# Performance work log

Hardware: AMD Instinct MI355X
Metric: run time of the kernel (lower is better)

The kernel has to match this reference:

```python
import jax, jax.numpy as jnp
import numpy as np

N = 50000        # nodes
E = 1600000      # edges (before self loops)
D_IN = 768       # roberta-base hidden size
SIZES = [256, 256]
NEG_SLOPE = 0.2
EPS = 1e-16


def setup_inputs() -> dict:
    key = jax.random.key(0)
    ks = jax.random.split(key, 16)
    s = 0.05
    inp = {
        "x": jax.random.normal(ks[0], (N, D_IN), dtype=jnp.float32),
        "edge_index": jax.random.randint(ks[1], (2, E), 0, N, dtype=jnp.int64),
        # GAT layer 0
        "W0": jax.random.normal(ks[2], (D_IN, SIZES[0]), dtype=jnp.float32) * s,
        "a_src0": jax.random.normal(ks[3], (SIZES[0],), dtype=jnp.float32) * s,
        "a_dst0": jax.random.normal(ks[4], (SIZES[0],), dtype=jnp.float32) * s,
        "b0": jnp.zeros((SIZES[0],), dtype=jnp.float32),
        # GAT layer 1
        "W1": jax.random.normal(ks[5], (SIZES[0], SIZES[1]), dtype=jnp.float32) * s,
        "a_src1": jax.random.normal(ks[6], (SIZES[1],), dtype=jnp.float32) * s,
        "a_dst1": jax.random.normal(ks[7], (SIZES[1],), dtype=jnp.float32) * s,
        "b1": jnp.zeros((SIZES[1],), dtype=jnp.float32),
        # GlobalAttention gate_nn: Linear(256 -> 1)
        "gate_w": jax.random.normal(ks[8], (SIZES[1], 1), dtype=jnp.float32) * s,
        "gate_b": jnp.zeros((1,), dtype=jnp.float32),
    }
    return inp


def _gat_layer(x, src, dst, W, a_src, a_dst, b):
    # PyG GATConv, heads=1: h = x W; e_ij = leaky_relu(a_src.h_j + a_dst.h_i)
    # softmax over edges grouped by target node i, then weighted aggregation.
    h = x @ W                                   # [N, D]
    alpha_src = h @ a_src                       # [N]
    alpha_dst = h @ a_dst                       # [N]
    e = jax.nn.leaky_relu(alpha_src[src] + alpha_dst[dst], NEG_SLOPE)  # [E']
    e_max = jax.ops.segment_max(e, dst, num_segments=N)
    e = jnp.exp(e - e_max[dst])
    denom = jax.ops.segment_sum(e, dst, num_segments=N)
    alpha = e / (denom[dst] + EPS)              # [E'] softmax per target
    out = jax.ops.segment_sum(alpha[:, None] * h[src], dst, num_segments=N)
    return out + b


def reference(x, edge_index, W0, a_src0, a_dst0, b0, W1, a_src1, a_dst1, b1, gate_w, gate_b):
    # add self loops (GATConv default add_self_loops=True)
    loop = jnp.arange(N, dtype=edge_index.dtype)
    src = jnp.concatenate([edge_index[0], loop])
    dst = jnp.concatenate([edge_index[1], loop])

    h = jax.nn.relu(_gat_layer(x, src, dst, W0, a_src0, a_dst0, b0))
    h = jax.nn.relu(_gat_layer(h, src, dst, W1, a_src1, a_dst1, b1))

    # GlobalAttention pooling over the single graph
    gate = h @ gate_w + gate_b                  # [N, 1]
    attn = jax.nn.softmax(gate, axis=0)         # softmax over nodes
    out = jnp.sum(attn * h, axis=0, keepdims=True)  # [1, 256]
    return out
```

## Files before the change

kernel.cpp:

```cpp
#include <hip/hip_runtime.h>

typedef unsigned int uint;
typedef unsigned short u16;
typedef unsigned char u8;

typedef __attribute__((ext_vector_type(8))) short short8;
typedef __attribute__((ext_vector_type(8))) u16 u16x8;
typedef __attribute__((ext_vector_type(4))) float f32x4;
typedef __attribute__((ext_vector_type(2))) float f32x2;

#define NN 50000
#define EE 1600000
#define ETOT (EE + NN)
#define NBUCK 782
#define ACHUNK 8192
#define CAP 2432
#define NSLOT 64
#define SLOTW 260

__device__ __forceinline__ u16 f2bf(float f) {
  uint u = __builtin_bit_cast(uint, f);
  uint r = u + 0x7fffu + ((u >> 16) & 1u);
  return (u16)(r >> 16);
}
__device__ __forceinline__ float bf2f(u16 h) {
  return __builtin_bit_cast(float, ((uint)h) << 16);
}
__device__ __forceinline__ u8 f2fp8(float f) {
  int t = __builtin_amdgcn_cvt_pk_fp8_f32(f, f, 0, false);
  return (u8)(t & 0xff);
}
__device__ __forceinline__ float wred_sum(float v) {
#pragma unroll
  for (int off = 32; off > 0; off >>= 1) v += __shfl_xor(v, off);
  return v;
}

__global__ void zero_ws(uint* __restrict__ bnxt, float* __restrict__ slots) {
  int i = blockIdx.x * 256 + threadIdx.x;
  if (i < NBUCK) bnxt[i] = 0u;
  if (i < NSLOT * SLOTW) slots[i] = 0.f;
}

__global__ void wt_both(const float* __restrict__ W0, const float* __restrict__ W1,
                        u16* __restrict__ Wt0, u16* __restrict__ Wt1) {
  int i = blockIdx.x * 256 + threadIdx.x;
  if (i < 768 * 256) {
    int k = i >> 8, n = i & 255;
    Wt0[n * 768 + k] = f2bf(W0[i]);
  } else if (i < 768 * 256 + 256 * 256) {
    int j = i - 768 * 256;
    int k = j >> 8, n = j & 255;
    Wt1[n * 256 + k] = f2bf(W1[j]);
  }
}

template <bool ABF16>
__global__ __launch_bounds__(512) void gemm_fused(const void* __restrict__ Avoid,
                                                  const u16* __restrict__ Bt,
                                                  u8* __restrict__ C8,
                                                  const float* __restrict__ a_src,
                                                  const float* __restrict__ a_dst,
                                                  float* __restrict__ as_,
                                                  float* __restrict__ ad_,
                                                  int M, int K) {
  __shared__ __align__(16) u16 As[128 * 64];
  __shared__ __align__(16) u16 Bs[256 * 64];
  __shared__ float asLds[4][128];
  __shared__ float adLds[4][128];
  const int m0 = blockIdx.x * 128;
  const int tid = threadIdx.x;
  const int lane = tid & 63;
  const int wv = tid >> 6;
  const int wm = wv >> 2, wn = wv & 3;

  f32x4 acc[4][4] = {};

  const int sr = tid >> 2;
  const int skc = (tid & 3) * 16;
  const int br = tid >> 1;
  const int bk = (tid & 1) * 32;

  for (int k0 = 0; k0 < K; k0 += 64) {
    {
      int grow = m0 + sr;
      if constexpr (!ABF16) {
        const float* A = (const float*)Avoid;
        float4 f[4];
        if (grow < M) {
          const float4* src = reinterpret_cast<const float4*>(A + (size_t)grow * K + k0 + skc);
#pragma unroll
          for (int i = 0; i < 4; ++i) f[i] = src[i];
        } else {
#pragma unroll
          for (int i = 0; i < 4; ++i) f[i] = make_float4(0.f, 0.f, 0.f, 0.f);
        }
#pragma unroll
        for (int i = 0; i < 2; ++i) {
          u16x8 v;
          v[0] = f2bf(f[2 * i].x); v[1] = f2bf(f[2 * i].y);
          v[2] = f2bf(f[2 * i].z); v[3] = f2bf(f[2 * i].w);
          v[4] = f2bf(f[2 * i + 1].x); v[5] = f2bf(f[2 * i + 1].y);
          v[6] = f2bf(f[2 * i + 1].z); v[7] = f2bf(f[2 * i + 1].w);
          int k = skc + i * 8;
          int idx = (sr << 6) + (k ^ ((sr & 7) << 3));
          *reinterpret_cast<u16x8*>(&As[idx]) = v;
        }
      } else {
        const u16* A = (const u16*)Avoid;
        u16x8 v[2];
        if (grow < M) {
          const u16x8* src = reinterpret_cast<const u16x8*>(A + (size_t)grow * K + k0 + skc);
          v[0] = src[0]; v[1] = src[1];
        } else {
          v[0] = (u16x8)0; v[1] = (u16x8)0;
        }
#pragma unroll
        for (int i = 0; i < 2; ++i) {
          int k = skc + i * 8;
          int idx = (sr << 6) + (k ^ ((sr & 7) << 3));
          *reinterpret_cast<u16x8*>(&As[idx]) = v[i];
        }
      }
    }
    {
      const u16x8* src = reinterpret_cast<const u16x8*>(Bt + (size_t)br * K + k0 + bk);
#pragma unroll
      for (int i = 0; i < 4; ++i) {
        u16x8 v = src[i];
        int k = bk + i * 8;
        int idx = (br << 6) + (k ^ ((br & 7) << 3));
        *reinterpret_cast<u16x8*>(&Bs[idx]) = v;
      }
    }
    __syncthreads();
#pragma unroll
    for (int kk = 0; kk < 2; ++kk) {
      short8 af[4], bfr[4];
      const int kb = kk * 32 + (lane >> 4) * 8;
#pragma unroll
      for (int m = 0; m < 4; ++m) {
        int r = wm * 64 + m * 16 + (lane & 15);
        int idx = (r << 6) + (kb ^ ((r & 7) << 3));
        af[m] = *reinterpret_cast<const short8*>(&As[idx]);
      }
#pragma unroll
      for (int n = 0; n < 4; ++n) {
        int c = wn * 64 + n * 16 + (lane & 15);
        int idx = (c << 6) + (kb ^ ((c & 7) << 3));
        bfr[n] = *reinterpret_cast<const short8*>(&Bs[idx]);
      }
#pragma unroll
      for (int m = 0; m < 4; ++m)
#pragma unroll
        for (int n = 0; n < 4; ++n)
          acc[m][n] = __builtin_amdgcn_mfma_f32_16x16x32_bf16(af[m], bfr[n], acc[m][n], 0, 0, 0);
    }
    __syncthreads();
  }

  const int g = lane >> 4;
  const int cl = lane & 15;
  float asv[4], adv[4];
#pragma unroll
  for (int n = 0; n < 4; ++n) {
    int c = wn * 64 + n * 16 + cl;
    asv[n] = a_src[c];
    adv[n] = a_dst[c];
  }
#pragma unroll
  for (int m = 0; m < 4; ++m) {
#pragma unroll
    for (int reg = 0; reg < 4; ++reg) {
      int rl = wm * 64 + m * 16 + g * 4 + reg;
      int row = m0 + rl;
      float ps = 0.f, pd = 0.f;
      if (row < M) {
#pragma unroll
        for (int n = 0; n < 4; ++n) {
          float v = acc[m][n][reg];
          C8[(size_t)row * 256 + wn * 64 + n * 16 + cl] = f2fp8(v);
          ps = fmaf(v, asv[n], ps);
          pd = fmaf(v, adv[n], pd);
        }
      }
#pragma unroll
      for (int off = 1; off < 16; off <<= 1) {
        ps += __shfl_xor(ps, off);
        pd += __shfl_xor(pd, off);
      }
      if (cl == 0) {
        asLds[wn][rl] = ps;
        adLds[wn][rl] = pd;
      }
    }
  }
  __syncthreads();
  if (tid < 128) {
    int row = m0 + tid;
    if (row < M) {
      as_[row] = asLds[0][tid] + asLds[1][tid] + asLds[2][tid] + asLds[3][tid];
      ad_[row] = adLds[0][tid] + adLds[1][tid] + adLds[2][tid] + adLds[3][tid];
    }
  }
}

__global__ __launch_bounds__(256) void bucket_scatter(const int* __restrict__ esrc,
                                                      const int* __restrict__ edst,
                                                      uint* __restrict__ bnxt,
                                                      uint* __restrict__ tmp) {
  __shared__ uint lh[NBUCK];
  int base = blockIdx.x * ACHUNK;
  int nE = ETOT - base; if (nE > ACHUNK) nE = ACHUNK;
  for (int i = threadIdx.x; i < NBUCK; i += 256) lh[i] = 0;
  __syncthreads();
  for (int k = threadIdx.x; k < nE; k += 256) {
    int e = base + k;
    int d = (e < EE) ? edst[e] : (e - EE);
    atomicAdd(&lh[d >> 6], 1u);
  }
  __syncthreads();
  for (int i = threadIdx.x; i < NBUCK; i += 256) {
    uint c = lh[i];
    lh[i] = c ? atomicAdd(&bnxt[i], c) : 0u;
  }
  __syncthreads();
  for (int k = threadIdx.x; k < nE; k += 256) {
    int e = base + k;
    int s, d;
    if (e < EE) { s = esrc[e]; d = edst[e]; } else { s = e - EE; d = s; }
    uint pos = atomicAdd(&lh[d >> 6], 1u);
    tmp[(size_t)(d >> 6) * CAP + pos] = ((uint)(d & 63) << 16) | (uint)s;
  }
}

__global__ __launch_bounds__(1024) void scanb_kernel(const uint* __restrict__ bnxt,
                                                     uint* __restrict__ bptr) {
  __shared__ uint wsum[16];
  int tid = threadIdx.x, lane = tid & 63, w = tid >> 6;
  uint v = (tid < NBUCK) ? bnxt[tid] : 0u;
  uint x = v;
#pragma unroll
  for (int off = 1; off < 64; off <<= 1) {
    uint t = __shfl_up(x, off);
    if (lane >= off) x += t;
  }
  if (lane == 63) wsum[w] = x;
  __syncthreads();
  uint woff = 0;
  for (int k = 0; k < w; ++k) woff += wsum[k];
  uint excl = woff + x - v;
  if (tid < NBUCK) bptr[tid] = excl;
}

__global__ __launch_bounds__(256) void bucket_sort(const uint* __restrict__ tmp,
                                                   const uint* __restrict__ bptr,
                                                   const uint* __restrict__ bnxt,
                                                   uint* __restrict__ row_ptr,
                                                   u16* __restrict__ csr) {
  __shared__ uint lh[64];
  __shared__ uint buf[CAP];
  int b = blockIdx.x;
  uint s0 = bptr[b];
  int cnt = (int)bnxt[b];
  int tid = threadIdx.x;
  if (tid < 64) lh[tid] = 0;
  __syncthreads();
  for (int i = tid; i < cnt; i += 256) {
    uint v = tmp[(size_t)b * CAP + i];
    buf[i] = v;
    atomicAdd(&lh[v >> 16], 1u);
  }
  __syncthreads();
  if (tid < 64) {
    uint v = lh[tid];
    uint x = v;
#pragma unroll
    for (int off = 1; off < 64; off <<= 1) {
      uint t = __shfl_up(x, off);
      if (tid >= off) x += t;
    }
    uint pos = s0 + x - v;
    int d = b * 64 + tid;
    if (d < NN) row_ptr[d] = pos;
    lh[tid] = pos;
    if (b == NBUCK - 1 && tid == 0) row_ptr[NN] = s0 + (uint)cnt;
  }
  __syncthreads();
  for (int i = tid; i < cnt; i += 256) {
    uint v = buf[i];
    uint pos = atomicAdd(&lh[v >> 16], 1u);
    csr[pos] = (u16)(v & 0xFFFFu);
  }
}

#define FMA16(v, wg)                                                                   \
  do {                                                                                 \
    f32x2 p_;                                                                          \
    p_ = __builtin_amdgcn_cvt_pk_f32_fp8((v).x, false);                                \
    acc[0] = fmaf((wg), p_.x, acc[0]); acc[1] = fmaf((wg), p_.y, acc[1]);              \
    p_ = __builtin_amdgcn_cvt_pk_f32_fp8((v).x, true);                                 \
    acc[2] = fmaf((wg), p_.x, acc[2]); acc[3] = fmaf((wg), p_.y, acc[3]);              \
    p_ = __builtin_amdgcn_cvt_pk_f32_fp8((v).y, false);                                \
    acc[4] = fmaf((wg), p_.x, acc[4]); acc[5] = fmaf((wg), p_.y, acc[5]);              \
    p_ = __builtin_amdgcn_cvt_pk_f32_fp8((v).y, true);                                 \
    acc[6] = fmaf((wg), p_.x, acc[6]); acc[7] = fmaf((wg), p_.y, acc[7]);              \
    p_ = __builtin_amdgcn_cvt_pk_f32_fp8((v).z, false);                                \
    acc[8] = fmaf((wg), p_.x, acc[8]); acc[9] = fmaf((wg), p_.y, acc[9]);              \
    p_ = __builtin_amdgcn_cvt_pk_f32_fp8((v).z, true);                                 \
    acc[10] = fmaf((wg), p_.x, acc[10]); acc[11] = fmaf((wg), p_.y, acc[11]);          \
    p_ = __builtin_amdgcn_cvt_pk_f32_fp8((v).w, false);                                \
    acc[12] = fmaf((wg), p_.x, acc[12]); acc[13] = fmaf((wg), p_.y, acc[13]);          \
    p_ = __builtin_amdgcn_cvt_pk_f32_fp8((v).w, true);                                 \
    acc[14] = fmaf((wg), p_.x, acc[14]); acc[15] = fmaf((wg), p_.y, acc[15]);          \
  } while (0)

template <bool POOL>
__global__ __launch_bounds__(256) void agg_kernel(const uint4* __restrict__ h16,
                                                  const float* __restrict__ as_,
                                                  const float* __restrict__ ad_,
                                                  const uint* __restrict__ row_ptr,
                                                  const u16* __restrict__ csr_src,
                                                  const float* __restrict__ bias,
                                                  u16* __restrict__ out,
                                                  const float* __restrict__ gate_w,
                                                  float* __restrict__ slots, int n) {
  __shared__ float tr[4][4][16][17];
  __shared__ float lp[257];
  int wv = threadIdx.x >> 6;
  int wid = blockIdx.x * 4 + wv;
  int lane = threadIdx.x & 63;
  int g = lane >> 4, li = lane & 15;
  if (POOL) {
    for (int i = threadIdx.x; i < 257; i += 256) lp[i] = 0.f;
    __syncthreads();
  }
  if (wid < n) {
    uint start = row_ptr[wid], end = row_ptr[wid + 1];
    float adi = ad_[wid];
    float acc[16];
#pragma unroll
    for (int c = 0; c < 16; ++c) acc[c] = 0.f;
    float denom = 0.f;
    for (uint base = start; base < end; base += 64) {
      int cnt = (int)(end - base);
      if (cnt > 64) cnt = 64;
      float w = 0.f;
      int s = 0;
      if (lane < cnt) {
        s = (int)csr_src[base + lane];
        float e = as_[s] + adi;
        e = e > 0.f ? e : 0.2f * e;
        w = __expf(e);
      }
      denom += w;
      int j = 0;
      for (; j + 16 <= cnt; j += 16) {
        int s0 = __shfl(s, j + g);
        int s1 = __shfl(s, j + 4 + g);
        int s2 = __shfl(s, j + 8 + g);
        int s3 = __shfl(s, j + 12 + g);
        float w0 = __shfl(w, j + g);
        float w1 = __shfl(w, j + 4 + g);
        float w2 = __shfl(w, j + 8 + g);
        float w3 = __shfl(w, j + 12 + g);
        uint4 v0 = h16[(size_t)s0 * 16 + li];
        uint4 v1 = h16[(size_t)s1 * 16 + li];
        uint4 v2 = h16[(size_t)s2 * 16 + li];
        uint4 v3 = h16[(size_t)s3 * 16 + li];
        FMA16(v0, w0);
        FMA16(v1, w1);
        FMA16(v2, w2);
        FMA16(v3, w3);
      }
      for (; j < cnt; j += 4) {
        int jg = j + g;
        int sg = __shfl(s, jg & 63);
        float wg = __shfl(w, jg & 63);
        if (jg >= cnt) wg = 0.f;
        uint4 v = h16[(size_t)sg * 16 + li];
        FMA16(v, wg);
      }
    }
    denom = wred_sum(denom);
#pragma unroll
    for (int c4 = 0; c4 < 4; ++c4)
      *reinterpret_cast<float4*>(&tr[wv][g][li][c4 * 4]) =
          make_float4(acc[c4 * 4], acc[c4 * 4 + 1], acc[c4 * 4 + 2], acc[c4 * 4 + 3]);
    asm volatile("s_waitcnt lgkmcnt(0)" ::: "memory");
    __builtin_amdgcn_sched_barrier(0);
    float ax = 0.f, ay = 0.f, az = 0.f, aw = 0.f;
#pragma unroll
    for (int gg = 0; gg < 4; ++gg) {
      const float* r = &tr[wv][gg][lane >> 2][4 * (lane & 3)];
      ax += r[0]; ay += r[1]; az += r[2]; aw += r[3];
    }
    float inv = 1.f / (denom + 1e-16f);
    float4 b = reinterpret_cast<const float4*>(bias)[lane];
    float ox = fmaxf(fmaf(ax, inv, b.x), 0.f);
    float oy = fmaxf(fmaf(ay, inv, b.y), 0.f);
    float oz = fmaxf(fmaf(az, inv, b.z), 0.f);
    float ow = fmaxf(fmaf(aw, inv, b.w), 0.f);
    if (!POOL) {
      ushort4 o;
      o.x = f2bf(ox); o.y = f2bf(oy); o.z = f2bf(oz); o.w = f2bf(ow);
      reinterpret_cast<ushort4*>(out)[(size_t)wid * 64 + lane] = o;
    } else {
      float4 gv = reinterpret_cast<const float4*>(gate_w)[lane];
      float pg = wred_sum(ox * gv.x + oy * gv.y + oz * gv.z + ow * gv.w);
      float we = __expf(pg);
      int c0 = lane * 4;
      atomicAdd(&lp[c0 + 0], we * ox);
      atomicAdd(&lp[c0 + 1], we * oy);
      atomicAdd(&lp[c0 + 2], we * oz);
      atomicAdd(&lp[c0 + 3], we * ow);
      if (lane == 0) atomicAdd(&lp[256], we);
    }
  }
  if (POOL) {
    __syncthreads();
    int slot = blockIdx.x & (NSLOT - 1);
    for (int i = threadIdx.x; i < 257; i += 256) {
      float v = lp[i];
      if (v != 0.f) atomicAdd(&slots[slot * SLOTW + i], v);
    }
  }
}

__global__ void pool3_kernel(const float* __restrict__ slots, float* __restrict__ out) {
  __shared__ float dsh;
  int tid = threadIdx.x;
  float acc = 0.f;
  for (int s = 0; s < NSLOT; ++s) acc += slots[s * SLOTW + tid];
  if (tid == 0) {
    float d = 0.f;
    for (int s = 0; s < NSLOT; ++s) d += slots[s * SLOTW + 256];
    dsh = d;
  }
  __syncthreads();
  out[tid] = acc / dsh;
}

extern "C" void kernel_launch(void* const* d_in, const int* in_sizes, int n_in,
                              void* d_out, int out_size, void* d_ws, size_t ws_size,
                              hipStream_t stream) {
  const float* x = (const float*)d_in[0];
  const int* edge = (const int*)d_in[1];
  const float* W0 = (const float*)d_in[2];
  const float* a_src0 = (const float*)d_in[3];
  const float* a_dst0 = (const float*)d_in[4];
  const float* b0 = (const float*)d_in[5];
  const float* W1 = (const float*)d_in[6];
  const float* a_src1 = (const float*)d_in[7];
  const float* a_dst1 = (const float*)d_in[8];
  const float* b1 = (const float*)d_in[9];
  const float* gate_w = (const float*)d_in[10];
  float* out = (float*)d_out;

  char* p = (char*)d_ws;
  size_t off = 0;
  auto take = [&](size_t bytes) -> char* {
    char* r = p + off;
    off = (off + bytes + 255) & ~(size_t)255;
    return r;
  };
  u8* hA = (u8*)take((size_t)NN * 256);
  u16* hB = (u16*)take((size_t)NN * 256 * 2);
  u16* Wt0 = (u16*)take((size_t)256 * 768 * 2);
  u16* Wt1 = (u16*)take((size_t)256 * 256 * 2);
  float* as0 = (float*)take((size_t)NN * 4);
  float* ad0 = (float*)take((size_t)NN * 4);
  float* as1 = (float*)take((size_t)NN * 4);
  float* ad1 = (float*)take((size_t)NN * 4);
  float* slots = (float*)take((size_t)NSLOT * SLOTW * 4);
  uint* bptr = (uint*)take((size_t)NBUCK * 4);
  uint* bnxt = (uint*)take((size_t)NBUCK * 4);
  uint* row_ptr = (uint*)take((size_t)(NN + 1) * 4);
  uint* tmp = (uint*)take((size_t)NBUCK * CAP * 4);
  u16* csr = (u16*)take((size_t)ETOT * 2);

  const int* edge_src = edge;
  const int* edge_dst = edge + EE;

  zero_ws<<<(NSLOT * SLOTW + 255) / 256, 256, 0, stream>>>(bnxt, slots);
  wt_both<<<1024, 256, 0, stream>>>(W0, W1, Wt0, Wt1);

  bucket_scatter<<<(ETOT + ACHUNK - 1) / ACHUNK, 256, 0, stream>>>(edge_src, edge_dst, bnxt, tmp);
  scanb_kernel<<<1, 1024, 0, stream>>>(bnxt, bptr);
  bucket_sort<<<NBUCK, 256, 0, stream>>>(tmp, bptr, bnxt, row_ptr, csr);

  const int ggrid = (NN + 127) / 128;
  gemm_fused<false><<<ggrid, 512, 0, stream>>>(x, Wt0, hA, a_src0, a_dst0, as0, ad0, NN, 768);
  agg_kernel<false><<<12500, 256, 0, stream>>>((const uint4*)hA, as0, ad0, row_ptr, csr, b0, hB,
                                               gate_w, slots, NN);
  gemm_fused<true><<<ggrid, 512, 0, stream>>>(hB, Wt1, hA, a_src1, a_dst1, as1, ad1, NN, 256);
  agg_kernel<true><<<12500, 256, 0, stream>>>((const uint4*)hA, as1, ad1, row_ptr, csr, b1, nullptr,
                                              gate_w, slots, NN);

  pool3_kernel<<<1, 256, 0, stream>>>(slots, out);
}
```

Measured before the change: 282.8 us.

## Merge preprocessing kernels and co-schedule bucket sort with first GEMM

Fuses the weight transpose into the edge bucket-scatter launch and removes the separate scan kernel: each sort block now computes its own bucket prefix by reducing all preceding bucket counts. The bucket-sort blocks are launched in the same grid as the layer-0 GEMM so both run concurrently, sharing one dynamically carved shared-memory buffer. This cuts kernel launches from 7 to 4 before aggregation and overlaps the sort with the GEMM. In exchange each sort block redundantly reads up to 782 counts, and the larger shared footprint of the GEMM block applies to sort blocks too.

```diff
diff --git a/kernel.cpp b/kernel.cpp
--- a/kernel.cpp
+++ b/kernel.cpp
@@ -14,18 +14,17 @@
 #define ETOT (EE + NN)
 #define NBUCK 782
 #define ACHUNK 8192
+#define NSC ((ETOT + ACHUNK - 1) / ACHUNK)
 #define CAP 2432
 #define NSLOT 64
 #define SLOTW 260
+#define GEMM_BLOCKS ((NN + 127) / 128)
 
 __device__ __forceinline__ u16 f2bf(float f) {
   uint u = __builtin_bit_cast(uint, f);
   uint r = u + 0x7fffu + ((u >> 16) & 1u);
   return (u16)(r >> 16);
 }
-__device__ __forceinline__ float bf2f(u16 h) {
-  return __builtin_bit_cast(float, ((uint)h) << 16);
-}
 __device__ __forceinline__ u8 f2fp8(float f) {
   int t = __builtin_amdgcn_cvt_pk_fp8_f32(f, f, 0, false);
   return (u8)(t & 0xff);
@@ -35,40 +34,75 @@
   for (int off = 32; off > 0; off >>= 1) v += __shfl_xor(v, off);
   return v;
 }
+__device__ __forceinline__ uint wred_sum_u(uint v) {
+#pragma unroll
+  for (int off = 32; off > 0; off >>= 1) v += __shfl_xor(v, off);
+  return v;
+}
 
 __global__ void zero_ws(uint* __restrict__ bnxt, float* __restrict__ slots) {
-  int i = blockIdx.x * 256 + threadIdx.x;
-  if (i < NBUCK) bnxt[i] = 0u;
-  if (i < NSLOT * SLOTW) slots[i] = 0.f;
-}
-
-__global__ void wt_both(const float* __restrict__ W0, const float* __restrict__ W1,
-                        u16* __restrict__ Wt0, u16* __restrict__ Wt1) {
-  int i = blockIdx.x * 256 + threadIdx.x;
-  if (i < 768 * 256) {
-    int k = i >> 8, n = i & 255;
-    Wt0[n * 768 + k] = f2bf(W0[i]);
-  } else if (i < 768 * 256 + 256 * 256) {
-    int j = i - 768 * 256;
-    int k = j >> 8, n = j & 255;
-    Wt1[n * 256 + k] = f2bf(W1[j]);
+  int t = threadIdx.x;
+  for (int i = t; i < NBUCK; i += 1024) bnxt[i] = 0u;
+  for (int i = t; i < NSLOT * SLOTW; i += 1024) slots[i] = 0.f;
+}
+
+__global__ __launch_bounds__(256) void scat_wt(const int* __restrict__ esrc,
+                                               const int* __restrict__ edst,
+                                               uint* __restrict__ bnxt,
+                                               uint* __restrict__ tmp,
+                                               const float* __restrict__ W0,
+                                               const float* __restrict__ W1,
+                                               u16* __restrict__ Wt0,
+                                               u16* __restrict__ Wt1) {
+  __shared__ uint lh[NBUCK];
+  if (blockIdx.x < NSC) {
+    int base = blockIdx.x * ACHUNK;
+    int nE = ETOT - base; if (nE > ACHUNK) nE = ACHUNK;
+    for (int i = threadIdx.x; i < NBUCK; i += 256) lh[i] = 0;
+    __syncthreads();
+    for (int k = threadIdx.x; k < nE; k += 256) {
+      int e = base + k;
+      int d = (e < EE) ? edst[e] : (e - EE);
+      atomicAdd(&lh[d >> 6], 1u);
+    }
+    __syncthreads();
+    for (int i = threadIdx.x; i < NBUCK; i += 256) {
+      uint c = lh[i];
+      lh[i] = c ? atomicAdd(&bnxt[i], c) : 0u;
+    }
+    __syncthreads();
+    for (int k = threadIdx.x; k < nE; k += 256) {
+      int e = base + k;
+      int s, d;
+      if (e < EE) { s = esrc[e]; d = edst[e]; } else { s = e - EE; d = s; }
+      uint pos = atomicAdd(&lh[d >> 6], 1u);
+      tmp[(size_t)(d >> 6) * CAP + pos] = ((uint)(d & 63) << 16) | (uint)s;
+    }
+  } else {
+    int i = (blockIdx.x - NSC) * 256 + threadIdx.x;
+    if (i < 768 * 256) {
+      int k = i >> 8, n = i & 255;
+      Wt0[n * 768 + k] = f2bf(W0[i]);
+    } else if (i < 768 * 256 + 256 * 256) {
+      int j = i - 768 * 256;
+      int k = j >> 8, n = j & 255;
+      Wt1[n * 256 + k] = f2bf(W1[j]);
+    }
   }
 }
 
 template <bool ABF16>
-__global__ __launch_bounds__(512) void gemm_fused(const void* __restrict__ Avoid,
-                                                  const u16* __restrict__ Bt,
-                                                  u8* __restrict__ C8,
-                                                  const float* __restrict__ a_src,
-                                                  const float* __restrict__ a_dst,
-                                                  float* __restrict__ as_,
-                                                  float* __restrict__ ad_,
-                                                  int M, int K) {
-  __shared__ __align__(16) u16 As[128 * 64];
-  __shared__ __align__(16) u16 Bs[256 * 64];
-  __shared__ float asLds[4][128];
-  __shared__ float adLds[4][128];
-  const int m0 = blockIdx.x * 128;
+__device__ __forceinline__ void gemm_body(char* smem, int bx, const void* __restrict__ Avoid,
+                                          const u16* __restrict__ Bt, u8* __restrict__ C8,
+                                          const float* __restrict__ a_src,
+                                          const float* __restrict__ a_dst,
+                                          float* __restrict__ as_, float* __restrict__ ad_,
+                                          int M, int K) {
+  u16* As = (u16*)smem;
+  u16* Bs = (u16*)(smem + 16384);
+  float* asL = (float*)(smem + 49152);
+  float* adL = (float*)(smem + 51200);
+  const int m0 = bx * 128;
   const int tid = threadIdx.x;
   const int lane = tid & 63;
   const int wv = tid >> 6;
@@ -190,8 +224,8 @@
         pd += __shfl_xor(pd, off);
       }
       if (cl == 0) {
-        asLds[wn][rl] = ps;
-        adLds[wn][rl] = pd;
+        asL[wn * 128 + rl] = ps;
+        adL[wn * 128 + rl] = pd;
       }
     }
   }
@@ -199,74 +233,31 @@
   if (tid < 128) {
     int row = m0 + tid;
     if (row < M) {
-      as_[row] = asLds[0][tid] + asLds[1][tid] + asLds[2][tid] + asLds[3][tid];
-      ad_[row] = adLds[0][tid] + adLds[1][tid] + adLds[2][tid] + adLds[3][tid];
-    }
-  }
-}
-
-__global__ __launch_bounds__(256) void bucket_scatter(const int* __restrict__ esrc,
-                                                      const int* __restrict__ edst,
-                                                      uint* __restrict__ bnxt,
-                                                      uint* __restrict__ tmp) {
-  __shared__ uint lh[NBUCK];
-  int base = blockIdx.x * ACHUNK;
-  int nE = ETOT - base; if (nE > ACHUNK) nE = ACHUNK;
-  for (int i = threadIdx.x; i < NBUCK; i += 256) lh[i] = 0;
-  __syncthreads();
-  for (int k = threadIdx.x; k < nE; k += 256) {
-    int e = base + k;
-    int d = (e < EE) ? edst[e] : (e - EE);
-    atomicAdd(&lh[d >> 6], 1u);
-  }
-  __syncthreads();
-  for (int i = threadIdx.x; i < NBUCK; i += 256) {
-    uint c = lh[i];
-    lh[i] = c ? atomicAdd(&bnxt[i], c) : 0u;
-  }
-  __syncthreads();
-  for (int k = threadIdx.x; k < nE; k += 256) {
-    int e = base + k;
-    int s, d;
-    if (e < EE) { s = esrc[e]; d = edst[e]; } else { s = e - EE; d = s; }
-    uint pos = atomicAdd(&lh[d >> 6], 1u);
-    tmp[(size_t)(d >> 6) * CAP + pos] = ((uint)(d & 63) << 16) | (uint)s;
-  }
-}
-
-__global__ __launch_bounds__(1024) void scanb_kernel(const uint* __restrict__ bnxt,
-                                                     uint* __restrict__ bptr) {
-  __shared__ uint wsum[16];
-  int tid = threadIdx.x, lane = tid & 63, w = tid >> 6;
-  uint v = (tid < NBUCK) ? bnxt[tid] : 0u;
-  uint x = v;
-#pragma unroll
-  for (int off = 1; off < 64; off <<= 1) {
-    uint t = __shfl_up(x, off);
-    if (lane >= off) x += t;
-  }
-  if (lane == 63) wsum[w] = x;
-  __syncthreads();
-  uint woff = 0;
-  for (int k = 0; k < w; ++k) woff += wsum[k];
-  uint excl = woff + x - v;
-  if (tid < NBUCK) bptr[tid] = excl;
-}
-
-__global__ __launch_bounds__(256) void bucket_sort(const uint* __restrict__ tmp,
-                                                   const uint* __restrict__ bptr,
-                                                   const uint* __restrict__ bnxt,
-                                                   uint* __restrict__ row_ptr,
-                                                   u16* __restrict__ csr) {
-  __shared__ uint lh[64];
-  __shared__ uint buf[CAP];
-  int b = blockIdx.x;
-  uint s0 = bptr[b];
+      as_[row] = asL[tid] + asL[128 + tid] + asL[256 + tid] + asL[384 + tid];
+      ad_[row] = adL[tid] + adL[128 + tid] + adL[256 + tid] + adL[384 + tid];
+    }
+  }
+}
+
+__device__ __forceinline__ void sort_body(char* smem, int b, const uint* __restrict__ tmp,
+                                          const uint* __restrict__ bnxt,
+                                          uint* __restrict__ row_ptr, u16* __restrict__ csr) {
+  uint* lh = (uint*)smem;
+  uint* red = (uint*)(smem + 256);
+  uint* buf = (uint*)(smem + 512);
+  int tid = threadIdx.x;
+  int lane = tid & 63, wv = tid >> 6;
+
+  uint part = 0;
+  for (int i = tid; i < b; i += 512) part += bnxt[i];
+  part = wred_sum_u(part);
+  if (lane == 0) red[wv] = part;
   int cnt = (int)bnxt[b];
-  int tid = threadIdx.x;
   if (tid < 64) lh[tid] = 0;
   __syncthreads();
-  for (int i = tid; i < cnt; i += 256) {
+  uint s0 = red[0] + red[1] + red[2] + red[3] + red[4] + red[5] + red[6] + red[7];
+
+  for (int i = tid; i < cnt; i += 512) {
     uint v = tmp[(size_t)b * CAP + i];
     buf[i] = v;
     atomicAdd(&lh[v >> 16], 1u);
@@ -287,10 +278,31 @@
     if (b == NBUCK - 1 && tid == 0) row_ptr[NN] = s0 + (uint)cnt;
   }
   __syncthreads();
-  for (int i = tid; i < cnt; i += 256) {
+  for (int i = tid; i < cnt; i += 512) {
     uint v = buf[i];
     uint pos = atomicAdd(&lh[v >> 16], 1u);
     csr[pos] = (u16)(v & 0xFFFFu);
+  }
+}
+
+template <bool ABF16>
+__global__ __launch_bounds__(512) void gemm_sort(const void* __restrict__ Avoid,
+                                                 const u16* __restrict__ Bt,
+                                                 u8* __restrict__ C8,
+                                                 const float* __restrict__ a_src,
+                                                 const float* __restrict__ a_dst,
+                                                 float* __restrict__ as_,
+                                                 float* __restrict__ ad_,
+                                                 int M, int K, int nsort,
+                                                 const uint* __restrict__ tmp,
+                                                 const uint* __restrict__ bnxt,
+                                                 uint* __restrict__ row_ptr,
+                                                 u16* __restrict__ csr) {
+  __shared__ __align__(16) char smem[53248];
+  if ((int)blockIdx.x < nsort) {
+    sort_body(smem, blockIdx.x, tmp, bnxt, row_ptr, csr);
+  } else {
+    gemm_body<ABF16>(smem, blockIdx.x - nsort, Avoid, Bt, C8, a_src, a_dst, as_, ad_, M, K);
   }
 }
 
@@ -473,7 +485,6 @@
   float* as1 = (float*)take((size_t)NN * 4);
   float* ad1 = (float*)take((size_t)NN * 4);
   float* slots = (float*)take((size_t)NSLOT * SLOTW * 4);
-  uint* bptr = (uint*)take((size_t)NBUCK * 4);
   uint* bnxt = (uint*)take((size_t)NBUCK * 4);
   uint* row_ptr = (uint*)take((size_t)(NN + 1) * 4);
   uint* tmp = (uint*)take((size_t)NBUCK * CAP * 4);
@@ -482,18 +493,15 @@
   const int* edge_src = edge;
   const int* edge_dst = edge + EE;
 
-  zero_ws<<<(NSLOT * SLOTW + 255) / 256, 256, 0, stream>>>(bnxt, slots);
-  wt_both<<<1024, 256, 0, stream>>>(W0, W1, Wt0, Wt1);
-
-  bucket_scatter<<<(ETOT + ACHUNK - 1) / ACHUNK, 256, 0, stream>>>(edge_src, edge_dst, bnxt, tmp);
-  scanb_kernel<<<1, 1024, 0, stream>>>(bnxt, bptr);
-  bucket_sort<<<NBUCK, 256, 0, stream>>>(tmp, bptr, bnxt, row_ptr, csr);
-
-  const int ggrid = (NN + 127) / 128;
-  gemm_fused<false><<<ggrid, 512, 0, stream>>>(x, Wt0, hA, a_src0, a_dst0, as0, ad0, NN, 768);
+  zero_ws<<<1, 1024, 0, stream>>>(bnxt, slots);
+  scat_wt<<<NSC + 1024, 256, 0, stream>>>(edge_src, edge_dst, bnxt, tmp, W0, W1, Wt0, Wt1);
+
+  gemm_sort<false><<<NBUCK + GEMM_BLOCKS, 512, 0, stream>>>(
+      x, Wt0, hA, a_src0, a_dst0, as0, ad0, NN, 768, NBUCK, tmp, bnxt, row_ptr, csr);
   agg_kernel<false><<<12500, 256, 0, stream>>>((const uint4*)hA, as0, ad0, row_ptr, csr, b0, hB,
                                                gate_w, slots, NN);
-  gemm_fused<true><<<ggrid, 512, 0, stream>>>(hB, Wt1, hA, a_src1, a_dst1, as1, ad1, NN, 256);
+  gemm_sort<true><<<GEMM_BLOCKS, 512, 0, stream>>>(
+      hB, Wt1, hA, a_src1, a_dst1, as1, ad1, NN, 256, 0, tmp, bnxt, row_ptr, csr);
   agg_kernel<true><<<12500, 256, 0, stream>>>((const uint4*)hA, as1, ad1, row_ptr, csr, b1, nullptr,
                                               gate_w, slots, NN);
 
```

After: 277.8 us (median of 2 runs). No clear change (-1.8%).
